# Kernel optimization log

Hardware: AMD Instinct MI355X
Metric: run time of the kernel (lower is better)

Reference implementation:

```python
import jax, jax.numpy as jnp
import numpy as np

E = 20000      # num edges
S = 64         # mul of 0e (scalar) channels
V = 32         # mul of 1o (vector) channels
FC_IN = 128    # radial basis length
HID = 64       # fc hidden width
INV_SQRT3 = 0.5773502691896258  # CG(1o x 1o -> 0e) = delta_ij / sqrt(3)


def setup_inputs() -> dict:
    key = jax.random.key(0)
    ks = jax.random.split(key, 16)
    n = jax.random.normal
    return {
        # edge features, layout [64 scalars | 32 vectors * 3 comps]
        "fea_in1": n(ks[0], (E, S + 3 * V), jnp.float32),
        "fea_in2": n(ks[1], (E, S + 3 * V), jnp.float32),
        "fea_weight": n(ks[2], (E, FC_IN), jnp.float32),
        # FullyConnectedTensorProduct internal weights (e3nn init: normal(0,1))
        "w_ss_s": n(ks[3], (S, S, S), jnp.float32),   # 0e x 0e -> 64x0e scalars
        "w_vv_s": n(ks[4], (V, V, S), jnp.float32),   # 1o x 1o -> 64x0e scalars
        "w_ss_g": n(ks[5], (S, S, V), jnp.float32),   # 0e x 0e -> 32x0e gates
        "w_vv_g": n(ks[6], (V, V, V), jnp.float32),   # 1o x 1o -> 32x0e gates
        "w_sv_v": n(ks[7], (S, V, V), jnp.float32),   # 0e x 1o -> 32x1o
        "w_vs_v": n(ks[8], (V, S, V), jnp.float32),   # 1o x 0e -> 32x1o
        # fc MLP: Linear(128,64) SiLU Linear(64,64) SiLU Linear(64,96)
        "fc_w1": n(ks[9], (FC_IN, HID), jnp.float32) / np.sqrt(FC_IN).astype(np.float32),
        "fc_b1": jnp.zeros((HID,), jnp.float32),
        "fc_w2": n(ks[10], (HID, HID), jnp.float32) / np.sqrt(HID).astype(np.float32),
        "fc_b2": jnp.zeros((HID,), jnp.float32),
        "fc_w3": n(ks[11], (HID, S + V), jnp.float32) / np.sqrt(HID).astype(np.float32),
        "fc_b3": jnp.zeros((S + V,), jnp.float32),
        "batch_edge": jnp.zeros((E,), jnp.int32),  # unused (norm='')
    }


def _equiconv(fea_in1, fea_in2, fea_weight,
              w_ss_s, w_vv_s, w_ss_g, w_vv_g, w_sv_v, w_vs_v,
              fc_w1, fc_b1, fc_w2, fc_b2, fc_w3, fc_b3):
    x1s, x1v = fea_in1[:, :S], fea_in1[:, S:].reshape(-1, V, 3)
    x2s, x2v = fea_in2[:, :S], fea_in2[:, S:].reshape(-1, V, 3)

    # path normalization: 1/sqrt(fan_in), fan_in = sum(mul1*mul2) over paths to output
    a_sc = 1.0 / np.sqrt(S * S + V * V).astype(np.float32)
    a_vec = 1.0 / np.sqrt(2 * S * V).astype(np.float32)

    # FullyConnectedTensorProduct (uvw connectivity)
    sc = a_sc * (jnp.einsum('eu,ev,uvw->ew', x1s, x2s, w_ss_s)
                 + INV_SQRT3 * jnp.einsum('eui,evi,uvw->ew', x1v, x2v, w_vv_s))
    g = a_sc * (jnp.einsum('eu,ev,uvw->ew', x1s, x2s, w_ss_g)
                + INV_SQRT3 * jnp.einsum('eui,evi,uvw->ew', x1v, x2v, w_vv_g))
    vec = a_vec * (jnp.einsum('eu,evi,uvw->ewi', x1s, x2v, w_sv_v)
                   + jnp.einsum('eui,ev,uvw->ewi', x1v, x2s, w_vs_v))

    # Gate: silu on scalars, sigmoid gates multiply the l>0 part
    sc = jax.nn.silu(sc)
    vec = vec * jax.nn.sigmoid(g)[:, :, None]

    # fc MLP producing per-channel elementwise conv weights
    h = jax.nn.silu(fea_weight @ fc_w1 + fc_b1)
    h = jax.nn.silu(h @ fc_w2 + fc_b2)
    w = h @ fc_w3 + fc_b3  # [E, S+V]

    # e3ElementWise: one scalar weight per channel (shared over m components)
    sc = sc * w[:, :S]
    vec = vec * w[:, S:, None]
    return jnp.concatenate([sc, vec.reshape(-1, 3 * V)], axis=-1)


def reference(fea_in1, fea_in2, fea_weight,
              w_ss_s, w_vv_s, w_ss_g, w_vv_g, w_sv_v, w_vs_v,
              fc_w1, fc_b1, fc_w2, fc_b2, fc_w3, fc_b3, batch_edge):
    del batch_edge  # only used by optional e3LayerNorm (norm='')
    return _equiconv(fea_in1, fea_in2, fea_weight,
                     w_ss_s, w_vv_s, w_ss_g, w_vv_g, w_sv_v, w_vs_v,
                     fc_w1, fc_b1, fc_w2, fc_b2, fc_w3, fc_b3)
```

## Files before the change

### kernel.cpp

```cpp
#include <hip/hip_runtime.h>


#define E_TOT 20000

typedef __attribute__((ext_vector_type(8))) short short8;
typedef __attribute__((ext_vector_type(4))) float f32x4;
typedef __attribute__((ext_vector_type(2))) __bf16 bf16x2;

#define FRAG_USH 512
#define CH_USH   3072
#define N_CH     52
#define STRIDE_W 159744
#define FC1_OFF  638976
#define FC2_OFF  647168
#define FC3_OFF  651264
#define WS_USH   657408

#define S_SSS 262144
#define O_SSG (S_SSS)
#define O_VVS (O_SSG+131072)
#define O_VVG (O_VVS+65536)
#define O_SV  (O_VVG+32768)
#define O_VS  (O_SV+65536)
#define O_F1  (O_VS+65536)
#define O_F2  (O_F1+8192)
#define O_F3  (O_F2+4096)
#define N_SRC (O_F3+6144)

__device__ __forceinline__ unsigned short f2b(float f){
  return __builtin_bit_cast(unsigned short, (__bf16)f);
}
__device__ __forceinline__ unsigned f2b2(float lo, float hi){
  bf16x2 t; t[0] = (__bf16)lo; t[1] = (__bf16)hi;
  return __builtin_bit_cast(unsigned, t);
}
__device__ __forceinline__ float b2f(unsigned short h){
  return __uint_as_float(((unsigned)h) << 16);
}
__device__ __forceinline__ f32x4 mfma16(short8 a, short8 b, f32x4 c){
  return __builtin_amdgcn_mfma_f32_16x16x32_bf16(a, b, c, 0, 0, 0);
}
union U8 { short8 v; unsigned u[4]; };
__device__ __forceinline__ float silu_f(float x){ return x/(1.f+__expf(-x)); }
__device__ __forceinline__ float sigm_f(float x){ return 1.f/(1.f+__expf(-x)); }

#define PACK8(a, s, x) \
  a.u[0]=f2b2((s)*(x)[0],(s)*(x)[1]); a.u[1]=f2b2((s)*(x)[2],(s)*(x)[3]); \
  a.u[2]=f2b2((s)*(x)[4],(s)*(x)[5]); a.u[3]=f2b2((s)*(x)[6],(s)*(x)[7]);

#define WAITV6 { __builtin_amdgcn_s_waitcnt(0xF76);  __builtin_amdgcn_sched_barrier(0); }
#define WAITV0 { __builtin_amdgcn_s_waitcnt(0xF70);  __builtin_amdgcn_sched_barrier(0); }
#define WAITL0 { __builtin_amdgcn_s_waitcnt(0xC07F); __builtin_amdgcn_sched_barrier(0); }

__device__ __forceinline__ int fpos(int kl, int n16){
  return (kl>>3)*128 + n16*8 + (kl&7);
}

__global__ void prep_weights(const float* __restrict__ ss_s, const float* __restrict__ ss_g,
                             const float* __restrict__ vv_s, const float* __restrict__ vv_g,
                             const float* __restrict__ sv,   const float* __restrict__ vs,
                             const float* __restrict__ w1,   const float* __restrict__ w2,
                             const float* __restrict__ w3,   unsigned short* __restrict__ wsb)
{
  int idx = blockIdx.x * 256 + threadIdx.x;
  if (idx >= N_SRC) return;
  const float A_SC  = 0.013975424859373686f;
  const float A_VV  = (float)(0.013975424859373686 * 0.5773502691896258);
  const float A_VEC = 0.015625f;
  float val; int dest;
  if (idx < O_SSG){
    int i = idx;
    int u = i >> 12, v = (i >> 6) & 63, w = i & 63;
    int wave = u >> 4, ul = u & 15;
    dest = wave*STRIDE_W + (ul*2 + (v>>5))*CH_USH + (w>>4)*FRAG_USH + fpos(v&31, w&15);
    val = A_SC * ss_s[i];
  } else if (idx < O_VVS){
    int i = idx - O_SSG;
    int u = i >> 11, v = (i >> 5) & 63, w = i & 31;
    int wave = u >> 4, ul = u & 15;
    dest = wave*STRIDE_W + (ul*2 + (v>>5))*CH_USH + (4+(w>>4))*FRAG_USH + fpos(v&31, w&15);
    val = A_SC * ss_g[i];
  } else if (idx < O_VVG){
    int i = idx - O_VVS;
    int u = i >> 11, v = (i >> 6) & 31, w = i & 63;
    int wave = u >> 3, ul = u & 7;
    dest = wave*STRIDE_W + (32+ul)*CH_USH + (w>>4)*FRAG_USH + fpos(v, w&15);
    val = A_VV * vv_s[i];
  } else if (idx < O_SV){
    int i = idx - O_VVG;
    int u = i >> 10, v = (i >> 5) & 31, w = i & 31;
    int wave = u >> 3, ul = u & 7;
    dest = wave*STRIDE_W + (32+ul)*CH_USH + (4+(w>>4))*FRAG_USH + fpos(v, w&15);
    val = A_VV * vv_g[i];
  } else if (idx < O_VS){
    int i = idx - O_SV;
    int u = i >> 10, v = (i >> 5) & 31, w = i & 31;
    int wave = u >> 4, ul = u & 15;
    dest = wave*STRIDE_W + (40 + ul/3)*CH_USH + ((ul%3)*2 + (w>>4))*FRAG_USH + fpos(v, w&15);
    val = A_VEC * sv[i];
  } else if (idx < O_F1){
    int i = idx - O_VS;
    int u = i >> 11, v = (i >> 5) & 63, w = i & 31;
    int wave = u >> 3, ul = u & 7;
    int fseq = ul*2 + (w>>4);
    dest = wave*STRIDE_W + (46 + (v>>5)*3 + fseq/6)*CH_USH + (fseq%6)*FRAG_USH + fpos(v&31, w&15);
    val = A_VEC * vs[i];
  } else if (idx < O_F2){
    int i = idx - O_F1;
    int k = i >> 6, n = i & 63;
    dest = FC1_OFF + ((k>>5)*4 + (n>>4))*FRAG_USH + fpos(k&31, n&15);
    val = w1[i];
  } else if (idx < O_F3){
    int i = idx - O_F2;
    int k = i >> 6, n = i & 63;
    dest = FC2_OFF + ((k>>5)*4 + (n>>4))*FRAG_USH + fpos(k&31, n&15);
    val = w2[i];
  } else {
    int i = idx - O_F3;
    int k = i / 96, n = i - k*96;
    dest = FC3_OFF + ((k>>5)*6 + (n>>4))*FRAG_USH + fpos(k&31, n&15);
    val = w3[i];
  }
  wsb[dest] = f2b(val);
}

__global__ __launch_bounds__(256, 2)
void equiconv_main(const float* __restrict__ fea1,
                   const float* __restrict__ fea2,
                   const float* __restrict__ few,
                   const float* __restrict__ fb1,
                   const float* __restrict__ fb2,
                   const float* __restrict__ fb3,
                   const unsigned short* __restrict__ wsb,
                   float* __restrict__ out)
{
  __shared__ __align__(16) unsigned short ring[4*2*CH_USH];
  __shared__ __align__(16) unsigned short x1s[32][66];
  __shared__ __align__(16) unsigned short x1v[32][98];
  __shared__ __align__(16) unsigned short hb[4][16][72];

  const int tid  = threadIdx.x;
  const int lane = tid & 63, wv = tid >> 6;
  const int ln   = lane & 15, quad = lane >> 4, q8 = quad << 3;
  const int ebase = blockIdx.x << 5;

  for (int it = tid; it < 1280; it += 256){
    int row = it / 40, seg = it - row*40;
    float4 v1 = *(const float4*)(fea1 + (size_t)(ebase + row)*160 + seg*4);
    const float* p1 = (const float*)&v1;
    int c0 = seg*4;
    #pragma unroll
    for (int jj = 0; jj < 4; jj++){
      int col = c0 + jj;
      if (col < 64) x1s[row][col] = f2b(p1[jj]);
      else          x1v[row][col-64] = f2b(p1[jj]);
    }
  }
  __syncthreads();

  float xe[2][8], xo[2][8], y0[2][8], y1[2][8], y2[2][8];
  #pragma unroll
  for (int s = 0; s < 2; s++){
    const float* p = fea2 + (size_t)(ebase + s*16 + ln)*160;
    float4 a0 = *(const float4*)(p + q8);
    float4 a1 = *(const float4*)(p + q8 + 4);
    float4 b0 = *(const float4*)(p + 32 + q8);
    float4 b1 = *(const float4*)(p + 36 + q8);
    xe[s][0]=a0.x; xe[s][1]=a0.y; xe[s][2]=a0.z; xe[s][3]=a0.w;
    xe[s][4]=a1.x; xe[s][5]=a1.y; xe[s][6]=a1.z; xe[s][7]=a1.w;
    xo[s][0]=b0.x; xo[s][1]=b0.y; xo[s][2]=b0.z; xo[s][3]=b0.w;
    xo[s][4]=b1.x; xo[s][5]=b1.y; xo[s][6]=b1.z; xo[s][7]=b1.w;
    const float* py = p + 64 + q8*3;
    float yb[24];
    #pragma unroll
    for (int t = 0; t < 12; t++){
      float2 f2v = *(const float2*)(py + 2*t);
      yb[2*t] = f2v.x; yb[2*t+1] = f2v.y;
    }
    #pragma unroll
    for (int j = 0; j < 8; j++){
      y0[s][j] = yb[3*j]; y1[s][j] = yb[3*j+1]; y2[s][j] = yb[3*j+2];
    }
  }

  const unsigned short* gstream = wsb + (size_t)wv*STRIDE_W;
  const int rbase = wv*2*CH_USH;
  auto issue_chunk = [&](int c){
    const unsigned short* g = gstream + c*CH_USH + lane*8;
    unsigned short* l = &ring[rbase + (c&1)*CH_USH];
    #pragma unroll
    for (int q = 0; q < 6; q++)
      __builtin_amdgcn_global_load_lds(
        (const __attribute__((address_space(1))) unsigned int*)(g + q*FRAG_USH),
        (__attribute__((address_space(3))) unsigned int*)(l + q*FRAG_USH),
        16, 0, 0);
  };
  issue_chunk(0); issue_chunk(1);

  const int r0 = ln, r1 = 16 + ln;
  const f32x4 z4 = {0.f,0.f,0.f,0.f};
  f32x4 accS[2][6] = {{z4,z4,z4,z4,z4,z4},{z4,z4,z4,z4,z4,z4}};
  f32x4 accV[2][3][2] = {{{z4,z4},{z4,z4},{z4,z4}},{{z4,z4},{z4,z4},{z4,z4}}};

  #define READ6(c, bb) { \
    const unsigned short* sl = &ring[rbase + ((c)&1)*CH_USH + lane*8]; \
    _Pragma("unroll") for (int t = 0; t < 6; t++) bb[t] = *(const short8*)(sl + t*FRAG_USH); }
  #define STEP(c) { WAITL0; if ((c)+2 < N_CH) issue_chunk((c)+2); }

  #pragma unroll 2
  for (int c = 0; c < 32; c++){
    int u = (wv<<4) + (c>>1);
    float s0 = b2f(x1s[r0][u]);
    float s1 = b2f(x1s[r1][u]);
    WAITV6;
    short8 bb[6]; READ6(c, bb); STEP(c);
    U8 a0, a1;
    if (c & 1){ PACK8(a0, s0, xo[0]); PACK8(a1, s1, xo[1]); }
    else      { PACK8(a0, s0, xe[0]); PACK8(a1, s1, xe[1]); }
    #pragma unroll
    for (int t = 0; t < 6; t++){
      accS[0][t] = mfma16(a0.v, bb[t], accS[0][t]);
      accS[1][t] = mfma16(a1.v, bb[t], accS[1][t]);
    }
  }
  #pragma unroll 1
  for (int k8 = 0; k8 < 8; k8++){
    int c = 32 + k8, u = (wv<<3) + k8;
    U8 a[2];
    #pragma unroll
    for (int s = 0; s < 2; s++){
      int rr = s ? r1 : r0;
      float c0 = b2f(x1v[rr][u*3+0]);
      float c1 = b2f(x1v[rr][u*3+1]);
      float c2 = b2f(x1v[rr][u*3+2]);
      float pv[8];
      #pragma unroll
      for (int j = 0; j < 8; j++)
        pv[j] = c0*y0[s][j] + c1*y1[s][j] + c2*y2[s][j];
      a[s].u[0]=f2b2(pv[0],pv[1]); a[s].u[1]=f2b2(pv[2],pv[3]);
      a[s].u[2]=f2b2(pv[4],pv[5]); a[s].u[3]=f2b2(pv[6],pv[7]);
    }
    WAITV6;
    short8 bb[6]; READ6(c, bb); STEP(c);
    #pragma unroll
    for (int t = 0; t < 6; t++){
      accS[0][t] = mfma16(a[0].v, bb[t], accS[0][t]);
      accS[1][t] = mfma16(a[1].v, bb[t], accS[1][t]);
    }
  }
  #pragma unroll 1
  for (int ch = 0; ch < 6; ch++){
    int c = 40 + ch;
    WAITV6;
    short8 bb[6]; READ6(c, bb); STEP(c);
    #pragma unroll
    for (int uu = 0; uu < 3; uu++){
      int ui = ch*3 + uu;
      if (ui < 16){
        int u = (wv<<4) + ui;
        float s0 = b2f(x1s[r0][u]);
        float s1 = b2f(x1s[r1][u]);
        U8 a[2][3];
        PACK8(a[0][0], s0, y0[0]); PACK8(a[0][1], s0, y1[0]); PACK8(a[0][2], s0, y2[0]);
        PACK8(a[1][0], s1, y0[1]); PACK8(a[1][1], s1, y1[1]); PACK8(a[1][2], s1, y2[1]);
        #pragma unroll
        for (int t = 0; t < 2; t++){
          short8 b8 = bb[uu*2 + t];
          #pragma unroll
          for (int s = 0; s < 2; s++)
            #pragma unroll
            for (int i = 0; i < 3; i++)
              accV[s][i][t] = mfma16(a[s][i].v, b8, accV[s][i][t]);
        }
      }
    }
  }
  #pragma unroll 1
  for (int pc = 0; pc < 6; pc++){
    int p = pc / 3, ch = pc - p*3;
    int c = 46 + pc;
    if (pc < 5) { WAITV6 }
    else        { WAITV0 }
    short8 bb[6]; READ6(c, bb); STEP(c);
    #pragma unroll
    for (int uu = 0; uu < 3; uu++){
      int ui = ch*3 + uu;
      if (ui < 8){
        int u = (wv<<3) + ui;
        U8 a[2][3];
        #pragma unroll
        for (int s = 0; s < 2; s++){
          int rr = s ? r1 : r0;
          float c0 = b2f(x1v[rr][u*3+0]);
          float c1 = b2f(x1v[rr][u*3+1]);
          float c2 = b2f(x1v[rr][u*3+2]);
          const float* xx = p ? xo[s] : xe[s];
          PACK8(a[s][0], c0, xx); PACK8(a[s][1], c1, xx); PACK8(a[s][2], c2, xx);
        }
        #pragma unroll
        for (int t = 0; t < 2; t++){
          short8 b8 = bb[uu*2 + t];
          #pragma unroll
          for (int s = 0; s < 2; s++)
            #pragma unroll
            for (int i = 0; i < 3; i++)
              accV[s][i][t] = mfma16(a[s][i].v, b8, accV[s][i][t]);
        }
      }
    }
  }

  f32x4 T0[12], T1[12];
  #pragma unroll
  for (int t = 0; t < 6; t++){ T0[t] = accS[0][t]; T1[t] = accS[1][t]; }
  #pragma unroll
  for (int t = 0; t < 2; t++)
    #pragma unroll
    for (int i = 0; i < 3; i++){
      T0[6+3*t+i] = accV[0][i][t]; T1[6+3*t+i] = accV[1][i][t];
    }

  float* redf = (float*)ring;
  #define PUT12(base, T) { _Pragma("unroll") for (int j=0;j<12;j++) \
    *(f32x4*)(redf + ((base)+j)*320 + ln*20 + (quad<<2)) = T[j]; }
  #define ADD12(base, T) { _Pragma("unroll") for (int j=0;j<12;j++) \
    T[j] += *(const f32x4*)(redf + ((base)+j)*320 + ln*20 + (quad<<2)); }

  __syncthreads();
  if (wv==1) PUT12(0, T0);  if (wv==2) PUT12(12, T1);
  __syncthreads();
  if (wv==0) ADD12(0, T0);  if (wv==3) ADD12(12, T1);
  __syncthreads();
  if (wv==2) PUT12(0, T0);  if (wv==1) PUT12(12, T1);
  __syncthreads();
  if (wv==0) ADD12(0, T0);  if (wv==3) ADD12(12, T1);
  __syncthreads();
  if (wv==3) PUT12(0, T0);  if (wv==0) PUT12(12, T1);
  __syncthreads();
  if (wv==0) ADD12(0, T0);  if (wv==3) ADD12(12, T1);

  if (wv == 1 || wv == 2) return;
  const int s = (wv == 0) ? 0 : 1;
  f32x4* P = (wv == 0) ? T0 : T1;

  f32x4 accF[4] = {z4,z4,z4,z4};
  {
    const float* fwp = few + (size_t)(ebase + s*16 + ln)*128;
    const short8* B = (const short8*)(wsb + FC1_OFF);
    #pragma unroll
    for (int c = 0; c < 4; c++){
      float4 fa  = *(const float4*)(fwp + c*32 + q8);
      float4 fbv = *(const float4*)(fwp + c*32 + q8 + 4);
      U8 a;
      a.u[0]=f2b2(fa.x,fa.y);   a.u[1]=f2b2(fa.z,fa.w);
      a.u[2]=f2b2(fbv.x,fbv.y); a.u[3]=f2b2(fbv.z,fbv.w);
      #pragma unroll
      for (int t = 0; t < 4; t++) accF[t] = mfma16(a.v, B[(c*4+t)*64 + lane], accF[t]);
    }
  }
  #pragma unroll
  for (int t = 0; t < 4; t++){
    float bb = fb1[(t<<4)+ln];
    #pragma unroll
    for (int r = 0; r < 4; r++)
      hb[wv][(quad<<2)+r][(t<<4)+ln] = f2b(silu_f(accF[t][r] + bb));
  }
  f32x4 acc2[4] = {z4,z4,z4,z4};
  {
    const short8* B = (const short8*)(wsb + FC2_OFF);
    #pragma unroll
    for (int c = 0; c < 2; c++){
      uint4 hq = *(const uint4*)&hb[wv][ln][c*32 + q8];
      U8 a; a.u[0]=hq.x; a.u[1]=hq.y; a.u[2]=hq.z; a.u[3]=hq.w;
      #pragma unroll
      for (int t = 0; t < 4; t++) acc2[t] = mfma16(a.v, B[(c*4+t)*64 + lane], acc2[t]);
    }
  }
  #pragma unroll
  for (int t = 0; t < 4; t++){
    float bb = fb2[(t<<4)+ln];
    #pragma unroll
    for (int r = 0; r < 4; r++)
      hb[wv][(quad<<2)+r][(t<<4)+ln] = f2b(silu_f(acc2[t][r] + bb));
  }
  f32x4 acc3[6] = {z4,z4,z4,z4,z4,z4};
  {
    const short8* B = (const short8*)(wsb + FC3_OFF);
    #pragma unroll
    for (int c = 0; c < 2; c++){
      uint4 hq = *(const uint4*)&hb[wv][ln][c*32 + q8];
      U8 a; a.u[0]=hq.x; a.u[1]=hq.y; a.u[2]=hq.z; a.u[3]=hq.w;
      #pragma unroll
      for (int t = 0; t < 6; t++) acc3[t] = mfma16(a.v, B[(c*6+t)*64 + lane], acc3[t]);
    }
  }

  #pragma unroll
  for (int r = 0; r < 4; r++){
    int eg = ebase + s*16 + (quad<<2) + r;
    float* op = out + (size_t)eg*160;
    #pragma unroll
    for (int t = 0; t < 4; t++)
      op[(t<<4)+ln] = silu_f(P[t][r]) * (acc3[t][r] + fb3[(t<<4)+ln]);
    #pragma unroll
    for (int tp = 0; tp < 2; tp++){
      int wc = (tp<<4) + ln;
      float f = sigm_f(P[4+tp][r]) * (acc3[4+tp][r] + fb3[64+wc]);
      op[64 + wc*3 + 0] = P[6+3*tp+0][r] * f;
      op[64 + wc*3 + 1] = P[6+3*tp+1][r] * f;
      op[64 + wc*3 + 2] = P[6+3*tp+2][r] * f;
    }
  }
}

extern "C" void kernel_launch(void* const* d_in, const int* in_sizes, int n_in,
                              void* d_out, int out_size, void* d_ws, size_t ws_size,
                              hipStream_t stream) {
  (void)in_sizes; (void)n_in; (void)out_size; (void)ws_size;
  unsigned short* wsb = (unsigned short*)d_ws;

  prep_weights<<<(N_SRC + 255)/256, 256, 0, stream>>>(
      (const float*)d_in[3], (const float*)d_in[5],
      (const float*)d_in[4], (const float*)d_in[6],
      (const float*)d_in[7], (const float*)d_in[8],
      (const float*)d_in[9], (const float*)d_in[11], (const float*)d_in[13],
      wsb);

  equiconv_main<<<E_TOT/32, 256, 0, stream>>>(
      (const float*)d_in[0], (const float*)d_in[1], (const float*)d_in[2],
      (const float*)d_in[10], (const float*)d_in[12], (const float*)d_in[14],
      (const unsigned short*)wsb, (float*)d_out);
}
```

Measured before the change: 181.0 us.

## Switch to 32x32x16 MFMA tiles and read weights directly from global

Reworks the main kernel to use 32x32x16 bf16 MFMA over all 32 edges per wave instead of two 16-row 16x16x32 tiles, with the weight layout repacked into 32-wide fragments. It drops the LDS ring and global_load_lds prefetch pipeline and loads B fragments straight from global memory, which likely hits in cache. The cross-wave reduction is simplified to a two-stage tree, and the MLP/output stage is split across two waves. The intent is fewer MFMA issues and less LDS traffic and synchronisation. The cost is higher register pressure from the 16-wide accumulators and exposed global load latency without explicit prefetch.

Measured after the change: 201.5 us. 11.3% more time.

```diff
diff --git a/kernel.cpp b/kernel.cpp
--- a/kernel.cpp
+++ b/kernel.cpp
@@ -5,19 +5,18 @@
 
 typedef __attribute__((ext_vector_type(8))) short short8;
 typedef __attribute__((ext_vector_type(4))) float f32x4;
+typedef __attribute__((ext_vector_type(16))) float f32x16;
 typedef __attribute__((ext_vector_type(2))) __bf16 bf16x2;
 
 #define FRAG_USH 512
-#define CH_USH   3072
-#define N_CH     52
-#define STRIDE_W 159744
-#define FC1_OFF  638976
-#define FC2_OFF  647168
-#define FC3_OFF  651264
-#define WS_USH   657408
-
-#define S_SSS 262144
-#define O_SSG (S_SSS)
+#define NFRAG_W  304
+#define STRIDE_W (NFRAG_W*FRAG_USH)
+#define FC1_OFF  (4*STRIDE_W)
+#define FC2_OFF  (FC1_OFF+8192)
+#define FC3_OFF  (FC2_OFF+4096)
+#define WS_USH   (FC3_OFF+6144)
+
+#define O_SSG 262144
 #define O_VVS (O_SSG+131072)
 #define O_VVG (O_VVS+65536)
 #define O_SV  (O_VVG+32768)
@@ -37,8 +36,8 @@
 __device__ __forceinline__ float b2f(unsigned short h){
   return __uint_as_float(((unsigned)h) << 16);
 }
-__device__ __forceinline__ f32x4 mfma16(short8 a, short8 b, f32x4 c){
-  return __builtin_amdgcn_mfma_f32_16x16x32_bf16(a, b, c, 0, 0, 0);
+__device__ __forceinline__ f32x16 mfma32(short8 a, short8 b, f32x16 c){
+  return __builtin_amdgcn_mfma_f32_32x32x16_bf16(a, b, c, 0, 0, 0);
 }
 union U8 { short8 v; unsigned u[4]; };
 __device__ __forceinline__ float silu_f(float x){ return x/(1.f+__expf(-x)); }
@@ -48,12 +47,10 @@
   a.u[0]=f2b2((s)*(x)[0],(s)*(x)[1]); a.u[1]=f2b2((s)*(x)[2],(s)*(x)[3]); \
   a.u[2]=f2b2((s)*(x)[4],(s)*(x)[5]); a.u[3]=f2b2((s)*(x)[6],(s)*(x)[7]);
 
-#define WAITV6 { __builtin_amdgcn_s_waitcnt(0xF76);  __builtin_amdgcn_sched_barrier(0); }
-#define WAITV0 { __builtin_amdgcn_s_waitcnt(0xF70);  __builtin_amdgcn_sched_barrier(0); }
-#define WAITL0 { __builtin_amdgcn_s_waitcnt(0xC07F); __builtin_amdgcn_sched_barrier(0); }
-
-__device__ __forceinline__ int fpos(int kl, int n16){
-  return (kl>>3)*128 + n16*8 + (kl&7);
+#define Z16(T) { _Pragma("unroll") for (int k_=0;k_<16;k_++) (T)[k_]=0.f; }
+
+__device__ __forceinline__ int fpos32(int kl, int n){
+  return ((kl>>3)*32 + n)*8 + (kl&7);
 }
 
 __global__ void prep_weights(const float* __restrict__ ss_s, const float* __restrict__ ss_g,
@@ -72,53 +69,58 @@
     int i = idx;
     int u = i >> 12, v = (i >> 6) & 63, w = i & 63;
     int wave = u >> 4, ul = u & 15;
-    dest = wave*STRIDE_W + (ul*2 + (v>>5))*CH_USH + (w>>4)*FRAG_USH + fpos(v&31, w&15);
+    int frag = ul*12 + (v>>4)*3 + (w>>5);
+    dest = wave*STRIDE_W + frag*FRAG_USH + fpos32(v&15, w&31);
     val = A_SC * ss_s[i];
   } else if (idx < O_VVS){
     int i = idx - O_SSG;
     int u = i >> 11, v = (i >> 5) & 63, w = i & 31;
     int wave = u >> 4, ul = u & 15;
-    dest = wave*STRIDE_W + (ul*2 + (v>>5))*CH_USH + (4+(w>>4))*FRAG_USH + fpos(v&31, w&15);
+    int frag = ul*12 + (v>>4)*3 + 2;
+    dest = wave*STRIDE_W + frag*FRAG_USH + fpos32(v&15, w);
     val = A_SC * ss_g[i];
   } else if (idx < O_VVG){
     int i = idx - O_VVS;
     int u = i >> 11, v = (i >> 6) & 31, w = i & 63;
     int wave = u >> 3, ul = u & 7;
-    dest = wave*STRIDE_W + (32+ul)*CH_USH + (w>>4)*FRAG_USH + fpos(v, w&15);
+    int frag = 192 + ul*6 + (v>>4)*3 + (w>>5);
+    dest = wave*STRIDE_W + frag*FRAG_USH + fpos32(v&15, w&31);
     val = A_VV * vv_s[i];
   } else if (idx < O_SV){
     int i = idx - O_VVG;
     int u = i >> 10, v = (i >> 5) & 31, w = i & 31;
     int wave = u >> 3, ul = u & 7;
-    dest = wave*STRIDE_W + (32+ul)*CH_USH + (4+(w>>4))*FRAG_USH + fpos(v, w&15);
+    int frag = 192 + ul*6 + (v>>4)*3 + 2;
+    dest = wave*STRIDE_W + frag*FRAG_USH + fpos32(v&15, w);
     val = A_VV * vv_g[i];
   } else if (idx < O_VS){
     int i = idx - O_SV;
     int u = i >> 10, v = (i >> 5) & 31, w = i & 31;
     int wave = u >> 4, ul = u & 15;
-    dest = wave*STRIDE_W + (40 + ul/3)*CH_USH + ((ul%3)*2 + (w>>4))*FRAG_USH + fpos(v, w&15);
+    int frag = 240 + ul*2 + (v>>4);
+    dest = wave*STRIDE_W + frag*FRAG_USH + fpos32(v&15, w);
     val = A_VEC * sv[i];
   } else if (idx < O_F1){
     int i = idx - O_VS;
     int u = i >> 11, v = (i >> 5) & 63, w = i & 31;
     int wave = u >> 3, ul = u & 7;
-    int fseq = ul*2 + (w>>4);
-    dest = wave*STRIDE_W + (46 + (v>>5)*3 + fseq/6)*CH_USH + (fseq%6)*FRAG_USH + fpos(v&31, w&15);
+    int frag = 272 + ul*4 + (v>>4);
+    dest = wave*STRIDE_W + frag*FRAG_USH + fpos32(v&15, w);
     val = A_VEC * vs[i];
   } else if (idx < O_F2){
     int i = idx - O_F1;
     int k = i >> 6, n = i & 63;
-    dest = FC1_OFF + ((k>>5)*4 + (n>>4))*FRAG_USH + fpos(k&31, n&15);
+    dest = FC1_OFF + ((k>>4)*2 + (n>>5))*FRAG_USH + fpos32(k&15, n&31);
     val = w1[i];
   } else if (idx < O_F3){
     int i = idx - O_F2;
     int k = i >> 6, n = i & 63;
-    dest = FC2_OFF + ((k>>5)*4 + (n>>4))*FRAG_USH + fpos(k&31, n&15);
+    dest = FC2_OFF + ((k>>4)*2 + (n>>5))*FRAG_USH + fpos32(k&15, n&31);
     val = w2[i];
   } else {
     int i = idx - O_F3;
     int k = i / 96, n = i - k*96;
-    dest = FC3_OFF + ((k>>5)*6 + (n>>4))*FRAG_USH + fpos(k&31, n&15);
+    dest = FC3_OFF + ((k>>4)*3 + (n>>5))*FRAG_USH + fpos32(k&15, n&31);
     val = w3[i];
   }
   wsb[dest] = f2b(val);
@@ -134,14 +136,16 @@
                    const unsigned short* __restrict__ wsb,
                    float* __restrict__ out)
 {
-  __shared__ __align__(16) unsigned short ring[4*2*CH_USH];
   __shared__ __align__(16) unsigned short x1s[32][66];
   __shared__ __align__(16) unsigned short x1v[32][98];
-  __shared__ __align__(16) unsigned short hb[4][16][72];
+  __shared__ __align__(16) unsigned short hb[2][32][72];
+  __shared__ __align__(16) float redf[12*1024];
 
   const int tid  = threadIdx.x;
   const int lane = tid & 63, wv = tid >> 6;
-  const int ln   = lane & 15, quad = lane >> 4, q8 = quad << 3;
+  const int n    = lane & 31;
+  const int kh   = lane >> 5;
+  const int ko   = kh << 3;
   const int ebase = blockIdx.x << 5;
 
   for (int it = tid; it < 1280; it += 256){
@@ -158,257 +162,202 @@
   }
   __syncthreads();
 
-  float xe[2][8], xo[2][8], y0[2][8], y1[2][8], y2[2][8];
+  float xq[4][8];
+  float yv[3][2][8];
+  {
+    const float* p = fea2 + (size_t)(ebase + n)*160;
+    #pragma unroll
+    for (int q = 0; q < 4; q++){
+      float4 a0 = *(const float4*)(p + q*16 + ko);
+      float4 a1 = *(const float4*)(p + q*16 + ko + 4);
+      xq[q][0]=a0.x; xq[q][1]=a0.y; xq[q][2]=a0.z; xq[q][3]=a0.w;
+      xq[q][4]=a1.x; xq[q][5]=a1.y; xq[q][6]=a1.z; xq[q][7]=a1.w;
+    }
+    #pragma unroll
+    for (int q = 0; q < 2; q++){
+      float yb[24];
+      const float* py = p + 64 + (q*16 + ko)*3;
+      #pragma unroll
+      for (int t = 0; t < 6; t++){
+        float4 f4 = *(const float4*)(py + 4*t);
+        yb[4*t]=f4.x; yb[4*t+1]=f4.y; yb[4*t+2]=f4.z; yb[4*t+3]=f4.w;
+      }
+      #pragma unroll
+      for (int j = 0; j < 8; j++){
+        yv[0][q][j] = yb[3*j]; yv[1][q][j] = yb[3*j+1]; yv[2][q][j] = yb[3*j+2];
+      }
+    }
+  }
+
+  f32x16 T[6];
   #pragma unroll
-  for (int s = 0; s < 2; s++){
-    const float* p = fea2 + (size_t)(ebase + s*16 + ln)*160;
-    float4 a0 = *(const float4*)(p + q8);
-    float4 a1 = *(const float4*)(p + q8 + 4);
-    float4 b0 = *(const float4*)(p + 32 + q8);
-    float4 b1 = *(const float4*)(p + 36 + q8);
-    xe[s][0]=a0.x; xe[s][1]=a0.y; xe[s][2]=a0.z; xe[s][3]=a0.w;
-    xe[s][4]=a1.x; xe[s][5]=a1.y; xe[s][6]=a1.z; xe[s][7]=a1.w;
-    xo[s][0]=b0.x; xo[s][1]=b0.y; xo[s][2]=b0.z; xo[s][3]=b0.w;
-    xo[s][4]=b1.x; xo[s][5]=b1.y; xo[s][6]=b1.z; xo[s][7]=b1.w;
-    const float* py = p + 64 + q8*3;
-    float yb[24];
-    #pragma unroll
-    for (int t = 0; t < 12; t++){
-      float2 f2v = *(const float2*)(py + 2*t);
-      yb[2*t] = f2v.x; yb[2*t+1] = f2v.y;
-    }
-    #pragma unroll
-    for (int j = 0; j < 8; j++){
-      y0[s][j] = yb[3*j]; y1[s][j] = yb[3*j+1]; y2[s][j] = yb[3*j+2];
-    }
-  }
-
-  const unsigned short* gstream = wsb + (size_t)wv*STRIDE_W;
-  const int rbase = wv*2*CH_USH;
-  auto issue_chunk = [&](int c){
-    const unsigned short* g = gstream + c*CH_USH + lane*8;
-    unsigned short* l = &ring[rbase + (c&1)*CH_USH];
-    #pragma unroll
-    for (int q = 0; q < 6; q++)
-      __builtin_amdgcn_global_load_lds(
-        (const __attribute__((address_space(1))) unsigned int*)(g + q*FRAG_USH),
-        (__attribute__((address_space(3))) unsigned int*)(l + q*FRAG_USH),
-        16, 0, 0);
-  };
-  issue_chunk(0); issue_chunk(1);
-
-  const int r0 = ln, r1 = 16 + ln;
-  const f32x4 z4 = {0.f,0.f,0.f,0.f};
-  f32x4 accS[2][6] = {{z4,z4,z4,z4,z4,z4},{z4,z4,z4,z4,z4,z4}};
-  f32x4 accV[2][3][2] = {{{z4,z4},{z4,z4},{z4,z4}},{{z4,z4},{z4,z4},{z4,z4}}};
-
-  #define READ6(c, bb) { \
-    const unsigned short* sl = &ring[rbase + ((c)&1)*CH_USH + lane*8]; \
-    _Pragma("unroll") for (int t = 0; t < 6; t++) bb[t] = *(const short8*)(sl + t*FRAG_USH); }
-  #define STEP(c) { WAITL0; if ((c)+2 < N_CH) issue_chunk((c)+2); }
+  for (int j = 0; j < 6; j++) Z16(T[j]);
+
+  const short8* G = (const short8*)(wsb + (size_t)wv*STRIDE_W);
 
   #pragma unroll 2
-  for (int c = 0; c < 32; c++){
-    int u = (wv<<4) + (c>>1);
-    float s0 = b2f(x1s[r0][u]);
-    float s1 = b2f(x1s[r1][u]);
-    WAITV6;
-    short8 bb[6]; READ6(c, bb); STEP(c);
-    U8 a0, a1;
-    if (c & 1){ PACK8(a0, s0, xo[0]); PACK8(a1, s1, xo[1]); }
-    else      { PACK8(a0, s0, xe[0]); PACK8(a1, s1, xe[1]); }
-    #pragma unroll
-    for (int t = 0; t < 6; t++){
-      accS[0][t] = mfma16(a0.v, bb[t], accS[0][t]);
-      accS[1][t] = mfma16(a1.v, bb[t], accS[1][t]);
-    }
-  }
-  #pragma unroll 1
-  for (int k8 = 0; k8 < 8; k8++){
-    int c = 32 + k8, u = (wv<<3) + k8;
-    U8 a[2];
-    #pragma unroll
-    for (int s = 0; s < 2; s++){
-      int rr = s ? r1 : r0;
-      float c0 = b2f(x1v[rr][u*3+0]);
-      float c1 = b2f(x1v[rr][u*3+1]);
-      float c2 = b2f(x1v[rr][u*3+2]);
+  for (int ul = 0; ul < 16; ul++){
+    float s = b2f(x1s[n][(wv<<4) + ul]);
+    #pragma unroll
+    for (int q = 0; q < 4; q++){
+      U8 a; PACK8(a, s, xq[q]);
+      #pragma unroll
+      for (int t = 0; t < 3; t++)
+        T[t] = mfma32(a.v, G[(ul*12 + q*3 + t)*64 + lane], T[t]);
+    }
+  }
+  #pragma unroll 2
+  for (int ul = 0; ul < 8; ul++){
+    int u = (wv<<3) + ul;
+    float c0 = b2f(x1v[n][u*3+0]);
+    float c1 = b2f(x1v[n][u*3+1]);
+    float c2 = b2f(x1v[n][u*3+2]);
+    #pragma unroll
+    for (int q = 0; q < 2; q++){
       float pv[8];
       #pragma unroll
       for (int j = 0; j < 8; j++)
-        pv[j] = c0*y0[s][j] + c1*y1[s][j] + c2*y2[s][j];
-      a[s].u[0]=f2b2(pv[0],pv[1]); a[s].u[1]=f2b2(pv[2],pv[3]);
-      a[s].u[2]=f2b2(pv[4],pv[5]); a[s].u[3]=f2b2(pv[6],pv[7]);
-    }
-    WAITV6;
-    short8 bb[6]; READ6(c, bb); STEP(c);
-    #pragma unroll
-    for (int t = 0; t < 6; t++){
-      accS[0][t] = mfma16(a[0].v, bb[t], accS[0][t]);
-      accS[1][t] = mfma16(a[1].v, bb[t], accS[1][t]);
-    }
-  }
-  #pragma unroll 1
-  for (int ch = 0; ch < 6; ch++){
-    int c = 40 + ch;
-    WAITV6;
-    short8 bb[6]; READ6(c, bb); STEP(c);
-    #pragma unroll
-    for (int uu = 0; uu < 3; uu++){
-      int ui = ch*3 + uu;
-      if (ui < 16){
-        int u = (wv<<4) + ui;
-        float s0 = b2f(x1s[r0][u]);
-        float s1 = b2f(x1s[r1][u]);
-        U8 a[2][3];
-        PACK8(a[0][0], s0, y0[0]); PACK8(a[0][1], s0, y1[0]); PACK8(a[0][2], s0, y2[0]);
-        PACK8(a[1][0], s1, y0[1]); PACK8(a[1][1], s1, y1[1]); PACK8(a[1][2], s1, y2[1]);
-        #pragma unroll
-        for (int t = 0; t < 2; t++){
-          short8 b8 = bb[uu*2 + t];
-          #pragma unroll
-          for (int s = 0; s < 2; s++)
-            #pragma unroll
-            for (int i = 0; i < 3; i++)
-              accV[s][i][t] = mfma16(a[s][i].v, b8, accV[s][i][t]);
-        }
-      }
-    }
-  }
-  #pragma unroll 1
-  for (int pc = 0; pc < 6; pc++){
-    int p = pc / 3, ch = pc - p*3;
-    int c = 46 + pc;
-    if (pc < 5) { WAITV6 }
-    else        { WAITV0 }
-    short8 bb[6]; READ6(c, bb); STEP(c);
-    #pragma unroll
-    for (int uu = 0; uu < 3; uu++){
-      int ui = ch*3 + uu;
-      if (ui < 8){
-        int u = (wv<<3) + ui;
-        U8 a[2][3];
-        #pragma unroll
-        for (int s = 0; s < 2; s++){
-          int rr = s ? r1 : r0;
-          float c0 = b2f(x1v[rr][u*3+0]);
-          float c1 = b2f(x1v[rr][u*3+1]);
-          float c2 = b2f(x1v[rr][u*3+2]);
-          const float* xx = p ? xo[s] : xe[s];
-          PACK8(a[s][0], c0, xx); PACK8(a[s][1], c1, xx); PACK8(a[s][2], c2, xx);
-        }
-        #pragma unroll
-        for (int t = 0; t < 2; t++){
-          short8 b8 = bb[uu*2 + t];
-          #pragma unroll
-          for (int s = 0; s < 2; s++)
-            #pragma unroll
-            for (int i = 0; i < 3; i++)
-              accV[s][i][t] = mfma16(a[s][i].v, b8, accV[s][i][t]);
-        }
-      }
-    }
-  }
-
-  f32x4 T0[12], T1[12];
-  #pragma unroll
-  for (int t = 0; t < 6; t++){ T0[t] = accS[0][t]; T1[t] = accS[1][t]; }
-  #pragma unroll
-  for (int t = 0; t < 2; t++)
-    #pragma unroll
-    for (int i = 0; i < 3; i++){
-      T0[6+3*t+i] = accV[0][i][t]; T1[6+3*t+i] = accV[1][i][t];
-    }
-
-  float* redf = (float*)ring;
-  #define PUT12(base, T) { _Pragma("unroll") for (int j=0;j<12;j++) \
-    *(f32x4*)(redf + ((base)+j)*320 + ln*20 + (quad<<2)) = T[j]; }
-  #define ADD12(base, T) { _Pragma("unroll") for (int j=0;j<12;j++) \
-    T[j] += *(const f32x4*)(redf + ((base)+j)*320 + ln*20 + (quad<<2)); }
-
+        pv[j] = c0*yv[0][q][j] + c1*yv[1][q][j] + c2*yv[2][q][j];
+      U8 a;
+      a.u[0]=f2b2(pv[0],pv[1]); a.u[1]=f2b2(pv[2],pv[3]);
+      a.u[2]=f2b2(pv[4],pv[5]); a.u[3]=f2b2(pv[6],pv[7]);
+      #pragma unroll
+      for (int t = 0; t < 3; t++)
+        T[t] = mfma32(a.v, G[(192 + ul*6 + q*3 + t)*64 + lane], T[t]);
+    }
+  }
+  #pragma unroll 2
+  for (int ul = 0; ul < 16; ul++){
+    float s = b2f(x1s[n][(wv<<4) + ul]);
+    #pragma unroll
+    for (int q = 0; q < 2; q++){
+      short8 b = G[(240 + ul*2 + q)*64 + lane];
+      U8 a0, a1, a2;
+      PACK8(a0, s, yv[0][q]); PACK8(a1, s, yv[1][q]); PACK8(a2, s, yv[2][q]);
+      T[3] = mfma32(a0.v, b, T[3]);
+      T[4] = mfma32(a1.v, b, T[4]);
+      T[5] = mfma32(a2.v, b, T[5]);
+    }
+  }
+  #pragma unroll 2
+  for (int ul = 0; ul < 8; ul++){
+    int u = (wv<<3) + ul;
+    float c0 = b2f(x1v[n][u*3+0]);
+    float c1 = b2f(x1v[n][u*3+1]);
+    float c2 = b2f(x1v[n][u*3+2]);
+    #pragma unroll
+    for (int q = 0; q < 4; q++){
+      short8 b = G[(272 + ul*4 + q)*64 + lane];
+      U8 a0, a1, a2;
+      PACK8(a0, c0, xq[q]); PACK8(a1, c1, xq[q]); PACK8(a2, c2, xq[q]);
+      T[3] = mfma32(a0.v, b, T[3]);
+      T[4] = mfma32(a1.v, b, T[4]);
+      T[5] = mfma32(a2.v, b, T[5]);
+    }
+  }
+
+  #define PUTT(slot, Tt) { _Pragma("unroll") for (int k=0;k<4;k++){ \
+      f32x4 v_ = { (Tt)[4*k], (Tt)[4*k+1], (Tt)[4*k+2], (Tt)[4*k+3] }; \
+      *(f32x4*)(redf + (slot)*1024 + lane*16 + k*4) = v_; } }
+  #define ADDT(slot, Tt) { _Pragma("unroll") for (int k=0;k<4;k++){ \
+      f32x4 v_ = *(const f32x4*)(redf + (slot)*1024 + lane*16 + k*4); \
+      (Tt)[4*k]+=v_[0]; (Tt)[4*k+1]+=v_[1]; (Tt)[4*k+2]+=v_[2]; (Tt)[4*k+3]+=v_[3]; } }
+
+  if (wv == 2){ PUTT(0,T[0]); PUTT(1,T[1]); PUTT(2,T[2]); PUTT(3,T[3]); PUTT(4,T[4]); PUTT(5,T[5]); }
+  if (wv == 3){ PUTT(6,T[0]); PUTT(7,T[1]); PUTT(8,T[2]); PUTT(9,T[3]); PUTT(10,T[4]); PUTT(11,T[5]); }
   __syncthreads();
-  if (wv==1) PUT12(0, T0);  if (wv==2) PUT12(12, T1);
+  if (wv == 0){ ADDT(0,T[0]); ADDT(1,T[1]); ADDT(2,T[2]); ADDT(3,T[3]); ADDT(4,T[4]); ADDT(5,T[5]); }
+  if (wv == 1){ ADDT(6,T[0]); ADDT(7,T[1]); ADDT(8,T[2]); ADDT(9,T[3]); ADDT(10,T[4]); ADDT(11,T[5]); }
   __syncthreads();
-  if (wv==0) ADD12(0, T0);  if (wv==3) ADD12(12, T1);
+  if (wv == 1){ PUTT(0,T[0]); PUTT(1,T[1]); }
+  if (wv == 0){ PUTT(2,T[2]); PUTT(3,T[3]); PUTT(4,T[4]); PUTT(5,T[5]); }
   __syncthreads();
-  if (wv==2) PUT12(0, T0);  if (wv==1) PUT12(12, T1);
-  __syncthreads();
-  if (wv==0) ADD12(0, T0);  if (wv==3) ADD12(12, T1);
-  __syncthreads();
-  if (wv==3) PUT12(0, T0);  if (wv==0) PUT12(12, T1);
-  __syncthreads();
-  if (wv==0) ADD12(0, T0);  if (wv==3) ADD12(12, T1);
-
-  if (wv == 1 || wv == 2) return;
-  const int s = (wv == 0) ? 0 : 1;
-  f32x4* P = (wv == 0) ? T0 : T1;
-
-  f32x4 accF[4] = {z4,z4,z4,z4};
+  if (wv == 0){ ADDT(0,T[0]); ADDT(1,T[1]); }
+  if (wv == 1){ ADDT(2,T[2]); ADDT(3,T[3]); ADDT(4,T[4]); ADDT(5,T[5]); }
+
+  if (wv >= 2) return;
+
+  f32x16 F0, F1;
+  Z16(F0); Z16(F1);
   {
-    const float* fwp = few + (size_t)(ebase + s*16 + ln)*128;
-    const short8* B = (const short8*)(wsb + FC1_OFF);
-    #pragma unroll
-    for (int c = 0; c < 4; c++){
-      float4 fa  = *(const float4*)(fwp + c*32 + q8);
-      float4 fbv = *(const float4*)(fwp + c*32 + q8 + 4);
+    const float* fp = few + (size_t)(ebase + n)*128;
+    const short8* B1 = (const short8*)(wsb + FC1_OFF);
+    #pragma unroll
+    for (int kc = 0; kc < 8; kc++){
+      float4 fa  = *(const float4*)(fp + kc*16 + ko);
+      float4 fbv = *(const float4*)(fp + kc*16 + ko + 4);
       U8 a;
       a.u[0]=f2b2(fa.x,fa.y);   a.u[1]=f2b2(fa.z,fa.w);
       a.u[2]=f2b2(fbv.x,fbv.y); a.u[3]=f2b2(fbv.z,fbv.w);
-      #pragma unroll
-      for (int t = 0; t < 4; t++) accF[t] = mfma16(a.v, B[(c*4+t)*64 + lane], accF[t]);
+      F0 = mfma32(a.v, B1[(kc*2+0)*64 + lane], F0);
+      F1 = mfma32(a.v, B1[(kc*2+1)*64 + lane], F1);
     }
   }
   #pragma unroll
-  for (int t = 0; t < 4; t++){
-    float bb = fb1[(t<<4)+ln];
-    #pragma unroll
-    for (int r = 0; r < 4; r++)
-      hb[wv][(quad<<2)+r][(t<<4)+ln] = f2b(silu_f(accF[t][r] + bb));
-  }
-  f32x4 acc2[4] = {z4,z4,z4,z4};
+  for (int t = 0; t < 2; t++){
+    float bb = fb1[t*32 + n];
+    const f32x16& F = t ? F1 : F0;
+    #pragma unroll
+    for (int r = 0; r < 16; r++){
+      int row = (r&3) + 8*(r>>2) + 4*kh;
+      hb[wv][row][t*32 + n] = f2b(silu_f(F[r] + bb));
+    }
+  }
+  Z16(F0); Z16(F1);
   {
-    const short8* B = (const short8*)(wsb + FC2_OFF);
-    #pragma unroll
-    for (int c = 0; c < 2; c++){
-      uint4 hq = *(const uint4*)&hb[wv][ln][c*32 + q8];
+    const short8* B2 = (const short8*)(wsb + FC2_OFF);
+    #pragma unroll
+    for (int kc = 0; kc < 4; kc++){
+      uint4 hq = *(const uint4*)&hb[wv][n][kc*16 + ko];
       U8 a; a.u[0]=hq.x; a.u[1]=hq.y; a.u[2]=hq.z; a.u[3]=hq.w;
-      #pragma unroll
-      for (int t = 0; t < 4; t++) acc2[t] = mfma16(a.v, B[(c*4+t)*64 + lane], acc2[t]);
+      F0 = mfma32(a.v, B2[(kc*2+0)*64 + lane], F0);
+      F1 = mfma32(a.v, B2[(kc*2+1)*64 + lane], F1);
     }
   }
   #pragma unroll
-  for (int t = 0; t < 4; t++){
-    float bb = fb2[(t<<4)+ln];
-    #pragma unroll
-    for (int r = 0; r < 4; r++)
-      hb[wv][(quad<<2)+r][(t<<4)+ln] = f2b(silu_f(acc2[t][r] + bb));
-  }
-  f32x4 acc3[6] = {z4,z4,z4,z4,z4,z4};
+  for (int t = 0; t < 2; t++){
+    float bb = fb2[t*32 + n];
+    const f32x16& F = t ? F1 : F0;
+    #pragma unroll
+    for (int r = 0; r < 16; r++){
+      int row = (r&3) + 8*(r>>2) + 4*kh;
+      hb[wv][row][t*32 + n] = f2b(silu_f(F[r] + bb));
+    }
+  }
+  f32x16 W0, W1, W2;
+  Z16(W0); Z16(W1); Z16(W2);
   {
-    const short8* B = (const short8*)(wsb + FC3_OFF);
-    #pragma unroll
-    for (int c = 0; c < 2; c++){
-      uint4 hq = *(const uint4*)&hb[wv][ln][c*32 + q8];
+    const short8* B3 = (const short8*)(wsb + FC3_OFF);
+    #pragma unroll
+    for (int kc = 0; kc < 4; kc++){
+      uint4 hq = *(const uint4*)&hb[wv][n][kc*16 + ko];
       U8 a; a.u[0]=hq.x; a.u[1]=hq.y; a.u[2]=hq.z; a.u[3]=hq.w;
-      #pragma unroll
-      for (int t = 0; t < 6; t++) acc3[t] = mfma16(a.v, B[(c*6+t)*64 + lane], acc3[t]);
-    }
-  }
-
-  #pragma unroll
-  for (int r = 0; r < 4; r++){
-    int eg = ebase + s*16 + (quad<<2) + r;
-    float* op = out + (size_t)eg*160;
-    #pragma unroll
-    for (int t = 0; t < 4; t++)
-      op[(t<<4)+ln] = silu_f(P[t][r]) * (acc3[t][r] + fb3[(t<<4)+ln]);
-    #pragma unroll
-    for (int tp = 0; tp < 2; tp++){
-      int wc = (tp<<4) + ln;
-      float f = sigm_f(P[4+tp][r]) * (acc3[4+tp][r] + fb3[64+wc]);
-      op[64 + wc*3 + 0] = P[6+3*tp+0][r] * f;
-      op[64 + wc*3 + 1] = P[6+3*tp+1][r] * f;
-      op[64 + wc*3 + 2] = P[6+3*tp+2][r] * f;
+      W0 = mfma32(a.v, B3[(kc*3+0)*64 + lane], W0);
+      W1 = mfma32(a.v, B3[(kc*3+1)*64 + lane], W1);
+      W2 = mfma32(a.v, B3[(kc*3+2)*64 + lane], W2);
+    }
+  }
+
+  if (wv == 0){
+    #pragma unroll
+    for (int r = 0; r < 16; r++){
+      int row = (r&3) + 8*(r>>2) + 4*kh;
+      float* op = out + (size_t)(ebase + row)*160;
+      float w0v = W0[r] + fb3[n];
+      float w1v = W1[r] + fb3[32 + n];
+      op[n]      = silu_f(T[0][r]) * w0v;
+      op[32 + n] = silu_f(T[1][r]) * w1v;
+    }
+  } else {
+    #pragma unroll
+    for (int r = 0; r < 16; r++){
+      int row = (r&3) + 8*(r>>2) + 4*kh;
+      float* op = out + (size_t)(ebase + row)*160;
+      float wv3 = W2[r] + fb3[64 + n];
+      float f = sigm_f(T[2][r]) * wv3;
+      op[64 + n*3 + 0] = T[3][r] * f;
+      op[64 + n*3 + 1] = T[4][r] * f;
+      op[64 + n*3 + 2] = T[5][r] * f;
     }
   }
 }
```
